# Performance work log

Measured on AMD Instinct MI355X. Metric: run time of the kernel, lower is better.

The kernel has to match this reference:

```python
import jax, jax.numpy as jnp
import numpy as np

VOCAB, EMB, HID, FC1, NCLS = 32000, 2048, 2048, 256, 3
T, B = 256, 128


def setup_inputs() -> dict:
    key = jax.random.key(0)
    ks = jax.random.split(key, 10)
    s_e = 1.0  # torch Embedding default init N(0,1)
    s_h = 1.0 / np.sqrt(HID)
    s_f1 = 1.0 / np.sqrt(HID)
    s_f2 = 1.0 / np.sqrt(FC1)
    return {
        "x": jax.random.randint(ks[0], (T, B), 0, VOCAB, dtype=jnp.int64)
        if jax.config.jax_enable_x64 else jax.random.randint(ks[0], (T, B), 0, VOCAB, dtype=jnp.int32),
        "emb": jax.random.normal(ks[1], (VOCAB, EMB), dtype=jnp.float32) * s_e,
        "W_ih": jax.random.uniform(ks[2], (HID, EMB), jnp.float32, -s_h, s_h),
        "W_hh": jax.random.uniform(ks[3], (HID, HID), jnp.float32, -s_h, s_h),
        "b_ih": jax.random.uniform(ks[4], (HID,), jnp.float32, -s_h, s_h),
        "b_hh": jax.random.uniform(ks[5], (HID,), jnp.float32, -s_h, s_h),
        "fc1_w": jax.random.uniform(ks[6], (FC1, HID), jnp.float32, -s_f1, s_f1),
        "fc1_b": jax.random.uniform(ks[7], (FC1,), jnp.float32, -s_f1, s_f1),
        "fc2_w": jax.random.uniform(ks[8], (NCLS, FC1), jnp.float32, -s_f2, s_f2),
        "fc2_b": jax.random.uniform(ks[9], (NCLS,), jnp.float32, -s_f2, s_f2),
    }


def reference(x, emb, W_ih, W_hh, b_ih, b_hh, fc1_w, fc1_b, fc2_w, fc2_b):
    # Embedding: [T, B] -> [T, B, E]
    xe = emb[x]
    # Precompute input projections for all steps in one big GEMM: [T, B, H]
    xproj = jnp.einsum("tbe,he->tbh", xe, W_ih) + b_ih + b_hh
    h0 = jnp.zeros((x.shape[1], W_hh.shape[0]), dtype=xe.dtype)

    def step(h, xp_t):
        h = jnp.tanh(xp_t + h @ W_hh.T)
        return h, None

    h_last, _ = jax.lax.scan(step, h0, xproj)
    # MLP head: hidden -> 256 -> relu -> 3
    z = jax.nn.relu(h_last @ fc1_w.T + fc1_b)
    return z @ fc2_w.T + fc2_b
```

## Files before the change

kernel.cpp:

```cpp
#include <hip/hip_runtime.h>

typedef _Float16 half8 __attribute__((ext_vector_type(8)));
typedef _Float16 half4v __attribute__((ext_vector_type(4)));
typedef float float4v __attribute__((ext_vector_type(4)));

#define HID 2048
#define EMBD 2048
#define BATCH 128
#define TSTEPS 256
#define STEP ((size_t)BATCH * HID)
#define SENT 0xFFFFFFFFFFFFFFFFull

#define LDH(hp, j, hh) __hip_atomic_load((hp) + (j) * 8 + (hh), __ATOMIC_RELAXED, __HIP_MEMORY_SCOPE_AGENT)

__global__ __launch_bounds__(256) void cast_f16_kernel(const float* __restrict__ src,
                                                       _Float16* __restrict__ dst, int n) {
    int i = (blockIdx.x * 256 + threadIdx.x) * 4;
    int stride = gridDim.x * 256 * 4;
    for (; i < n; i += stride) {
        float4v v = *(const float4v*)(src + i);
        half4v h;
        h[0] = (_Float16)v[0]; h[1] = (_Float16)v[1];
        h[2] = (_Float16)v[2]; h[3] = (_Float16)v[3];
        *(half4v*)(dst + i) = h;
    }
}

__global__ __launch_bounds__(256) void bias_kernel(const float* __restrict__ a,
                                                   const float* __restrict__ b,
                                                   float* __restrict__ dst) {
    int i = blockIdx.x * 256 + threadIdx.x;
    if (i < HID) dst[i] = a[i] + b[i];
}

__global__ __launch_bounds__(256) void phaseA_kernel(const int* __restrict__ x,
                                                     const float* __restrict__ emb,
                                                     const _Float16* __restrict__ w16,
                                                     const float* __restrict__ bias,
                                                     _Float16* __restrict__ xbias) {
    __shared__ __align__(16) _Float16 As[128 * 64];
    __shared__ __align__(16) _Float16 Bs[128 * 64];

    const int tid = threadIdx.x;
    const int bx  = blockIdx.x;
    const int nt = bx & 15, mt = bx >> 4;
    const long m0 = (long)mt * 128;
    const long n0 = (long)nt * 128;
    const int lane = tid & 63, w = tid >> 6;
    const int ln15 = lane & 15, kg = lane >> 4;
    const int wr = (w >> 1) * 64, wc = (w & 1) * 64;

    int xr[4];
#pragma unroll
    for (int it = 0; it < 4; ++it) xr[it] = x[m0 + ((it * 256 + tid) >> 3)];

    float4v acc[4][4];
#pragma unroll
    for (int m = 0; m < 4; ++m)
#pragma unroll
        for (int n = 0; n < 4; ++n) acc[m][n] = (float4v){0.f, 0.f, 0.f, 0.f};

    for (int kt = 0; kt < 32; ++kt) {
        __syncthreads();
#pragma unroll
        for (int it = 0; it < 4; ++it) {
            int c = it * 256 + tid;
            const float* src = emb + (long)xr[it] * EMBD + kt * 64 + (c & 7) * 8;
            float4v v0 = *(const float4v*)src;
            float4v v1 = *(const float4v*)(src + 4);
            half8 hv;
#pragma unroll
            for (int q = 0; q < 4; ++q) { hv[q] = (_Float16)v0[q]; hv[4 + q] = (_Float16)v1[q]; }
            *(half8*)(&As[c * 8]) = hv;
        }
#pragma unroll
        for (int it = 0; it < 4; ++it) {
            int c = it * 256 + tid;
            const _Float16* src = w16 + (n0 + (c >> 3)) * (long)EMBD + kt * 64 + (c & 7) * 8;
            *(half8*)(&Bs[c * 8]) = *(const half8*)src;
        }
        __syncthreads();
#pragma unroll
        for (int kk = 0; kk < 2; ++kk) {
            half8 a[4], b[4];
#pragma unroll
            for (int m = 0; m < 4; ++m)
                a[m] = *(half8*)(&As[(wr + m * 16 + ln15) * 64 + kk * 32 + kg * 8]);
#pragma unroll
            for (int n = 0; n < 4; ++n)
                b[n] = *(half8*)(&Bs[(wc + n * 16 + ln15) * 64 + kk * 32 + kg * 8]);
#pragma unroll
            for (int m = 0; m < 4; ++m)
#pragma unroll
                for (int n = 0; n < 4; ++n)
                    acc[m][n] = __builtin_amdgcn_mfma_f32_16x16x32_f16(b[n], a[m], acc[m][n], 0, 0, 0);
        }
    }
#pragma unroll
    for (int m = 0; m < 4; ++m) {
        long mg = m0 + wr + m * 16 + ln15;
#pragma unroll
        for (int n = 0; n < 4; ++n) {
            int nb = (int)n0 + wc + n * 16 + kg * 4;
            float4v bv = *(const float4v*)(bias + nb);
            union { half4v h; unsigned long long u; } pk;
#pragma unroll
            for (int r = 0; r < 4; ++r) pk.h[r] = (_Float16)(acc[m][n][r] + bv[r]);
            *(unsigned long long*)(xbias + mg * HID + nb) = pk.u;
        }
    }
}

__global__ __launch_bounds__(256, 1) void scan_kernel(const _Float16* __restrict__ xbias,
                                                      const _Float16* __restrict__ whh,
                                                      _Float16* __restrict__ ring,
                                                      float* __restrict__ hlast) {
    __shared__ __align__(16) _Float16 Wl[32 * 2048];
    __shared__ float part[4][16 * 33];

    const int tid = threadIdx.x;
    const int bx = blockIdx.x;
    const int gid = bx & 3, sub = bx >> 2;
    const int m0 = gid * 32, n0 = sub * 32;
    const int lane = tid & 63, w = tid >> 6;
    const int ln15 = lane & 15, kg = lane >> 4;
    const int pr = w >> 1, kh = w & 1;

    for (int it = 0; it < 32; ++it) {
        int c = it * 256 + tid;
        int col = c >> 8, ch = c & 255;
        half8 v = *(const half8*)(whh + (long)(n0 + col) * HID + ch * 8);
        *(half8*)((char*)Wl + col * 4096 + ((ch * 16) ^ ((col & 7) << 4))) = v;
    }
    __syncthreads();

    const size_t arow = (size_t)(m0 + pr * 16 + ln15);
    const int wb0 = ln15 * 4096;
    const int wb1 = (16 + ln15) * 4096;
    const int swz = (ln15 & 7) << 4;
    const int kb = kh * 2048;
    const int rp = tid >> 7, ridx = tid & 127;
    const int rrow = ridx >> 3, rc4 = (ridx & 7) * 4;
    const size_t oidx = (size_t)(m0 + rp * 16 + rrow) * HID + n0 + rc4;

    for (int s = 0; s < TSTEPS; ++s) {
        half4v xpv = *(const half4v*)(xbias + (size_t)s * STEP + oidx);

        float4v acc0 = (float4v){0.f, 0.f, 0.f, 0.f};
        float4v acc1 = (float4v){0.f, 0.f, 0.f, 0.f};
        if (s > 0) {
            const unsigned long long* hp = (const unsigned long long*)
                (ring + (size_t)((s - 1) & 7) * STEP + arow * HID + kh * 1024 + kg * 8);
            unsigned long long va[8][2], vb[8][2];
#pragma unroll
            for (int q = 0; q < 8; ++q) { va[q][0] = LDH(hp, q, 0); va[q][1] = LDH(hp, q, 1); }
#pragma unroll
            for (int bt = 0; bt < 4; ++bt) {
                if (bt < 3) {
#pragma unroll
                    for (int q = 0; q < 8; ++q) {
                        int jn = (bt + 1) * 8 + q;
                        if (bt & 1) { va[q][0] = LDH(hp, jn, 0); va[q][1] = LDH(hp, jn, 1); }
                        else        { vb[q][0] = LDH(hp, jn, 0); vb[q][1] = LDH(hp, jn, 1); }
                    }
                }
#pragma unroll
                for (int q = 0; q < 8; ++q) {
                    int j = bt * 8 + q;
                    unsigned long long x0 = (bt & 1) ? vb[q][0] : va[q][0];
                    unsigned long long x1 = (bt & 1) ? vb[q][1] : va[q][1];
                    while (x0 == SENT || x1 == SENT) { x0 = LDH(hp, j, 0); x1 = LDH(hp, j, 1); }
                    union { unsigned long long u[2]; half8 h; } ua; ua.u[0] = x0; ua.u[1] = x1;
                    int k2 = kb + j * 64 + kg * 16;
                    half8 b0 = *(half8*)((char*)Wl + wb0 + (k2 ^ swz));
                    half8 b1 = *(half8*)((char*)Wl + wb1 + (k2 ^ swz));
                    acc0 = __builtin_amdgcn_mfma_f32_16x16x32_f16(ua.h, b0, acc0, 0, 0, 0);
                    acc1 = __builtin_amdgcn_mfma_f32_16x16x32_f16(ua.h, b1, acc1, 0, 0, 0);
                }
            }
#pragma unroll
            for (int r = 0; r < 4; ++r) {
                part[w][(kg * 4 + r) * 33 + ln15] = acc0[r];
                part[w][(kg * 4 + r) * 33 + 16 + ln15] = acc1[r];
            }
        }

        float s0 = 0.f, s1 = 0.f, s2 = 0.f, s3 = 0.f;
        if (s > 0) {
            __syncthreads();
            const float* p0 = &part[2 * rp][rrow * 33 + rc4];
            const float* p1 = &part[2 * rp + 1][rrow * 33 + rc4];
            s0 = p0[0] + p1[0]; s1 = p0[1] + p1[1];
            s2 = p0[2] + p1[2]; s3 = p0[3] + p1[3];
            __syncthreads();
        }
        float o0 = tanhf(s0 + (float)xpv[0]);
        float o1 = tanhf(s1 + (float)xpv[1]);
        float o2 = tanhf(s2 + (float)xpv[2]);
        float o3 = tanhf(s3 + (float)xpv[3]);

        asm volatile("s_waitcnt vmcnt(0)" ::: "memory");
        if (s < TSTEPS - 1) {
            union { half4v h; unsigned long long u; } pk;
            pk.h[0] = (_Float16)o0; pk.h[1] = (_Float16)o1;
            pk.h[2] = (_Float16)o2; pk.h[3] = (_Float16)o3;
            __hip_atomic_store((unsigned long long*)(ring + (size_t)(s & 7) * STEP + oidx),
                               pk.u, __ATOMIC_RELAXED, __HIP_MEMORY_SCOPE_AGENT);
            __hip_atomic_store((unsigned long long*)(ring + (size_t)((s + 4) & 7) * STEP + oidx),
                               SENT, __ATOMIC_RELAXED, __HIP_MEMORY_SCOPE_AGENT);
        } else {
            float4v f = {o0, o1, o2, o3};
            *(float4v*)(hlast + oidx) = f;
        }
    }
}

__global__ __launch_bounds__(64) void fc1_kernel(const float* __restrict__ hlast,
                                                 const float* __restrict__ w,
                                                 const float* __restrict__ b,
                                                 float* __restrict__ z) {
    int bb = blockIdx.x;
    int j = blockIdx.y * 64 + threadIdx.x;
    const float* hr = hlast + (long)bb * HID;
    const float* wr = w + (long)j * HID;
    float acc = 0.f;
    for (int k = 0; k < HID; k += 4) {
        float4v hv = *(const float4v*)(hr + k);
        float4v wv = *(const float4v*)(wr + k);
        acc += hv[0] * wv[0] + hv[1] * wv[1] + hv[2] * wv[2] + hv[3] * wv[3];
    }
    acc += b[j];
    z[bb * 256 + j] = fmaxf(acc, 0.f);
}

__global__ __launch_bounds__(256) void fc2_kernel(const float* __restrict__ z,
                                                  const float* __restrict__ w,
                                                  const float* __restrict__ b,
                                                  float* __restrict__ out) {
    __shared__ float red[4];
    int bb = blockIdx.x;
    int tid = threadIdx.x;
    float zv = z[bb * 256 + tid];
    for (int c = 0; c < 3; ++c) {
        float s = zv * w[c * 256 + tid];
        for (int off = 32; off > 0; off >>= 1) s += __shfl_down(s, off, 64);
        if ((tid & 63) == 0) red[tid >> 6] = s;
        __syncthreads();
        if (tid == 0) out[bb * 3 + c] = red[0] + red[1] + red[2] + red[3] + b[c];
        __syncthreads();
    }
}

extern "C" void kernel_launch(void* const* d_in, const int* in_sizes, int n_in,
                              void* d_out, int out_size, void* d_ws, size_t ws_size,
                              hipStream_t stream) {
    const int*   x    = (const int*)d_in[0];
    const float* emb  = (const float*)d_in[1];
    const float* Wih  = (const float*)d_in[2];
    const float* Whh  = (const float*)d_in[3];
    const float* bih  = (const float*)d_in[4];
    const float* bhh  = (const float*)d_in[5];
    const float* fc1w = (const float*)d_in[6];
    const float* fc1b = (const float*)d_in[7];
    const float* fc2w = (const float*)d_in[8];
    const float* fc2b = (const float*)d_in[9];
    float* out = (float*)d_out;

    char* ws = (char*)d_ws;
    size_t off = 0;
    _Float16* xbias = (_Float16*)(ws + off); off += (size_t)TSTEPS * BATCH * HID * 2;
    _Float16* wih16 = (_Float16*)(ws + off); off += (size_t)HID * EMBD * 2;
    _Float16* whh16 = (_Float16*)(ws + off); off += (size_t)HID * HID * 2;
    float*    bias  = (float*)(ws + off);    off += (size_t)HID * 4;
    _Float16* ring  = (_Float16*)(ws + off); off += 8 * STEP * 2;
    float*    hlast = (float*)(ws + off);    off += (size_t)BATCH * HID * 4;
    float*    z     = (float*)(ws + off);    off += (size_t)BATCH * 256 * 4;

    hipMemsetAsync(ring, 0xFF, 8 * STEP * 2, stream);

    cast_f16_kernel<<<4096, 256, 0, stream>>>(Wih, wih16, HID * EMBD);
    cast_f16_kernel<<<4096, 256, 0, stream>>>(Whh, whh16, HID * HID);
    bias_kernel<<<8, 256, 0, stream>>>(bih, bhh, bias);

    phaseA_kernel<<<4096, 256, 0, stream>>>(x, emb, wih16, bias, xbias);

    void* args[] = {(void*)&xbias, (void*)&whh16, (void*)&ring, (void*)&hlast};
    hipLaunchCooperativeKernel((const void*)scan_kernel, dim3(256), dim3(256), args, 0, stream);

    fc1_kernel<<<dim3(128, 4), 64, 0, stream>>>(hlast, fc1w, fc1b, z);
    fc2_kernel<<<BATCH, 256, 0, stream>>>(z, fc2w, fc2b, out);
}
```

Measured before the change: 3.012 ms.

## Replace sentinel-polled ring buffer with per-group step flags and in-place hidden states

The scan kernel no longer polls every loaded hidden-state word for a sentinel value in an 8-slot ring buffer. Each block now publishes a per-group step counter after a block barrier, and consumers spin on 32 flag words with sleep before issuing plain vector loads of h. Hidden states are written in place over the already-consumed xproj buffer, which removes the separate ring and the sentinel stores. Flag-based sync cuts per-element polling and atomic load traffic, at the cost of an extra barrier and a flag round-trip each step. With relaxed ordering only, there is a memory-ordering risk between the data stores and the flag store.

```diff
diff --git a/kernel.cpp b/kernel.cpp
--- a/kernel.cpp
+++ b/kernel.cpp
@@ -9,9 +9,6 @@
 #define BATCH 128
 #define TSTEPS 256
 #define STEP ((size_t)BATCH * HID)
-#define SENT 0xFFFFFFFFFFFFFFFFull
-
-#define LDH(hp, j, hh) __hip_atomic_load((hp) + (j) * 8 + (hh), __ATOMIC_RELAXED, __HIP_MEMORY_SCOPE_AGENT)
 
 __global__ __launch_bounds__(256) void cast_f16_kernel(const float* __restrict__ src,
                                                        _Float16* __restrict__ dst, int n) {
@@ -37,7 +34,7 @@
                                                      const float* __restrict__ emb,
                                                      const _Float16* __restrict__ w16,
                                                      const float* __restrict__ bias,
-                                                     _Float16* __restrict__ xbias) {
+                                                     _Float16* __restrict__ xproj) {
     __shared__ __align__(16) _Float16 As[128 * 64];
     __shared__ __align__(16) _Float16 Bs[128 * 64];
 
@@ -106,15 +103,15 @@
             union { half4v h; unsigned long long u; } pk;
 #pragma unroll
             for (int r = 0; r < 4; ++r) pk.h[r] = (_Float16)(acc[m][n][r] + bv[r]);
-            *(unsigned long long*)(xbias + mg * HID + nb) = pk.u;
-        }
-    }
-}
-
-__global__ __launch_bounds__(256, 1) void scan_kernel(const _Float16* __restrict__ xbias,
+            *(unsigned long long*)(xproj + mg * HID + nb) = pk.u;
+        }
+    }
+}
+
+__global__ __launch_bounds__(256, 1) void scan_kernel(_Float16* __restrict__ xb,
                                                       const _Float16* __restrict__ whh,
-                                                      _Float16* __restrict__ ring,
-                                                      float* __restrict__ hlast) {
+                                                      float* __restrict__ hlast,
+                                                      unsigned* __restrict__ flags) {
     __shared__ __align__(16) _Float16 Wl[32 * 2048];
     __shared__ float part[4][16 * 33];
 
@@ -134,9 +131,10 @@
     }
     __syncthreads();
 
+    unsigned* gfl = flags + gid * 64;
+    const unsigned long long* gfl64 = (const unsigned long long*)gfl;
     const size_t arow = (size_t)(m0 + pr * 16 + ln15);
-    const int wb0 = ln15 * 4096;
-    const int wb1 = (16 + ln15) * 4096;
+    const int wb0 = ln15 * 4096, wb1 = (16 + ln15) * 4096;
     const int swz = (ln15 & 7) << 4;
     const int kb = kh * 2048;
     const int rp = tid >> 7, ridx = tid & 127;
@@ -144,39 +142,35 @@
     const size_t oidx = (size_t)(m0 + rp * 16 + rrow) * HID + n0 + rc4;
 
     for (int s = 0; s < TSTEPS; ++s) {
-        half4v xpv = *(const half4v*)(xbias + (size_t)s * STEP + oidx);
+        unsigned long long xbits = __hip_atomic_load(
+            (const unsigned long long*)(xb + (size_t)(s + 1) * STEP + oidx),
+            __ATOMIC_RELAXED, __HIP_MEMORY_SCOPE_AGENT);
 
         float4v acc0 = (float4v){0.f, 0.f, 0.f, 0.f};
         float4v acc1 = (float4v){0.f, 0.f, 0.f, 0.f};
         if (s > 0) {
-            const unsigned long long* hp = (const unsigned long long*)
-                (ring + (size_t)((s - 1) & 7) * STEP + arow * HID + kh * 1024 + kg * 8);
-            unsigned long long va[8][2], vb[8][2];
-#pragma unroll
-            for (int q = 0; q < 8; ++q) { va[q][0] = LDH(hp, q, 0); va[q][1] = LDH(hp, q, 1); }
-#pragma unroll
-            for (int bt = 0; bt < 4; ++bt) {
-                if (bt < 3) {
-#pragma unroll
-                    for (int q = 0; q < 8; ++q) {
-                        int jn = (bt + 1) * 8 + q;
-                        if (bt & 1) { va[q][0] = LDH(hp, jn, 0); va[q][1] = LDH(hp, jn, 1); }
-                        else        { vb[q][0] = LDH(hp, jn, 0); vb[q][1] = LDH(hp, jn, 1); }
-                    }
+            for (;;) {
+                bool ok = true;
+                if (lane < 32) {
+                    unsigned long long v = __hip_atomic_load(gfl64 + lane,
+                                            __ATOMIC_RELAXED, __HIP_MEMORY_SCOPE_AGENT);
+                    ok = ((unsigned)v >= (unsigned)s) && ((unsigned)(v >> 32) >= (unsigned)s);
                 }
-#pragma unroll
-                for (int q = 0; q < 8; ++q) {
-                    int j = bt * 8 + q;
-                    unsigned long long x0 = (bt & 1) ? vb[q][0] : va[q][0];
-                    unsigned long long x1 = (bt & 1) ? vb[q][1] : va[q][1];
-                    while (x0 == SENT || x1 == SENT) { x0 = LDH(hp, j, 0); x1 = LDH(hp, j, 1); }
-                    union { unsigned long long u[2]; half8 h; } ua; ua.u[0] = x0; ua.u[1] = x1;
-                    int k2 = kb + j * 64 + kg * 16;
-                    half8 b0 = *(half8*)((char*)Wl + wb0 + (k2 ^ swz));
-                    half8 b1 = *(half8*)((char*)Wl + wb1 + (k2 ^ swz));
-                    acc0 = __builtin_amdgcn_mfma_f32_16x16x32_f16(ua.h, b0, acc0, 0, 0, 0);
-                    acc1 = __builtin_amdgcn_mfma_f32_16x16x32_f16(ua.h, b1, acc1, 0, 0, 0);
-                }
+                if (__all(ok)) break;
+                __builtin_amdgcn_s_sleep(2);
+            }
+            asm volatile("" ::: "memory");
+            __builtin_amdgcn_sched_barrier(0);
+
+            const _Float16* hrow = xb + (size_t)(s - 1) * STEP + arow * HID + kh * 1024;
+#pragma unroll
+            for (int j = 0; j < 32; ++j) {
+                half8 a = *(const half8*)(hrow + j * 32 + kg * 8);
+                int k2 = kb + j * 64 + kg * 16;
+                half8 b0 = *(half8*)((char*)Wl + wb0 + (k2 ^ swz));
+                half8 b1 = *(half8*)((char*)Wl + wb1 + (k2 ^ swz));
+                acc0 = __builtin_amdgcn_mfma_f32_16x16x32_f16(a, b0, acc0, 0, 0, 0);
+                acc1 = __builtin_amdgcn_mfma_f32_16x16x32_f16(a, b1, acc1, 0, 0, 0);
             }
 #pragma unroll
             for (int r = 0; r < 4; ++r) {
@@ -192,22 +186,23 @@
             const float* p1 = &part[2 * rp + 1][rrow * 33 + rc4];
             s0 = p0[0] + p1[0]; s1 = p0[1] + p1[1];
             s2 = p0[2] + p1[2]; s3 = p0[3] + p1[3];
-            __syncthreads();
-        }
-        float o0 = tanhf(s0 + (float)xpv[0]);
-        float o1 = tanhf(s1 + (float)xpv[1]);
-        float o2 = tanhf(s2 + (float)xpv[2]);
-        float o3 = tanhf(s3 + (float)xpv[3]);
-
-        asm volatile("s_waitcnt vmcnt(0)" ::: "memory");
+        }
+        union { unsigned long long u; half4v h; } xbv; xbv.u = xbits;
+        float o0 = tanhf(s0 + (float)xbv.h[0]);
+        float o1 = tanhf(s1 + (float)xbv.h[1]);
+        float o2 = tanhf(s2 + (float)xbv.h[2]);
+        float o3 = tanhf(s3 + (float)xbv.h[3]);
+
         if (s < TSTEPS - 1) {
             union { half4v h; unsigned long long u; } pk;
             pk.h[0] = (_Float16)o0; pk.h[1] = (_Float16)o1;
             pk.h[2] = (_Float16)o2; pk.h[3] = (_Float16)o3;
-            __hip_atomic_store((unsigned long long*)(ring + (size_t)(s & 7) * STEP + oidx),
+            __hip_atomic_store((unsigned long long*)(xb + (size_t)s * STEP + oidx),
                                pk.u, __ATOMIC_RELAXED, __HIP_MEMORY_SCOPE_AGENT);
-            __hip_atomic_store((unsigned long long*)(ring + (size_t)((s + 4) & 7) * STEP + oidx),
-                               SENT, __ATOMIC_RELAXED, __HIP_MEMORY_SCOPE_AGENT);
+            __syncthreads();
+            if (tid == 0)
+                __hip_atomic_store(&gfl[sub], (unsigned)(s + 1),
+                                   __ATOMIC_RELAXED, __HIP_MEMORY_SCOPE_AGENT);
         } else {
             float4v f = {o0, o1, o2, o3};
             *(float4v*)(hlast + oidx) = f;
@@ -268,23 +263,23 @@
 
     char* ws = (char*)d_ws;
     size_t off = 0;
-    _Float16* xbias = (_Float16*)(ws + off); off += (size_t)TSTEPS * BATCH * HID * 2;
+    _Float16* xb    = (_Float16*)(ws + off); off += 257 * STEP * 2;
     _Float16* wih16 = (_Float16*)(ws + off); off += (size_t)HID * EMBD * 2;
     _Float16* whh16 = (_Float16*)(ws + off); off += (size_t)HID * HID * 2;
     float*    bias  = (float*)(ws + off);    off += (size_t)HID * 4;
-    _Float16* ring  = (_Float16*)(ws + off); off += 8 * STEP * 2;
     float*    hlast = (float*)(ws + off);    off += (size_t)BATCH * HID * 4;
     float*    z     = (float*)(ws + off);    off += (size_t)BATCH * 256 * 4;
-
-    hipMemsetAsync(ring, 0xFF, 8 * STEP * 2, stream);
+    unsigned* flags = (unsigned*)(ws + off); off += 4 * 64 * 4;
+
+    hipMemsetAsync(flags, 0, 4 * 64 * 4, stream);
 
     cast_f16_kernel<<<4096, 256, 0, stream>>>(Wih, wih16, HID * EMBD);
     cast_f16_kernel<<<4096, 256, 0, stream>>>(Whh, whh16, HID * HID);
     bias_kernel<<<8, 256, 0, stream>>>(bih, bhh, bias);
 
-    phaseA_kernel<<<4096, 256, 0, stream>>>(x, emb, wih16, bias, xbias);
-
-    void* args[] = {(void*)&xbias, (void*)&whh16, (void*)&ring, (void*)&hlast};
+    phaseA_kernel<<<4096, 256, 0, stream>>>(x, emb, wih16, bias, xb + STEP);
+
+    void* args[] = {(void*)&xb, (void*)&whh16, (void*)&hlast, (void*)&flags};
     hipLaunchCooperativeKernel((const void*)scan_kernel, dim3(256), dim3(256), args, 0, stream);
 
     fc1_kernel<<<dim3(128, 4), 64, 0, stream>>>(hlast, fc1w, fc1b, z);
```

Result: faster. 2.532 ms (-16.0%).
